# Optimization experiments

Hardware: AMD Instinct MI355X
Metric: run time of the kernel (lower is better)

## Reference

```python
import jax, jax.numpy as jnp
import numpy as np

LENS = 0.4
DECAY = 0.2
THRESH = 0.2
LOG_SIG_MIN, LOG_SIG_MAX = -20.0, 2.0

# Surrogate-gradient spike: forward is heaviside, backward is rectangular window |x|<lens
@jax.custom_vjp
def act_fun(x):
    return (x > 0.0).astype(x.dtype)

def _act_fwd(x):
    return act_fun(x), x

def _act_bwd(x, g):
    return (g * (jnp.abs(x) < LENS).astype(g.dtype),)

act_fun.defvjp(_act_fwd, _act_bwd)


def _xavier(k, shape):
    fan_out, fan_in = shape
    lim = float(np.sqrt(6.0 / (fan_in + fan_out)))
    return jax.random.uniform(k, shape, jnp.float32, -lim, lim)


def setup_inputs() -> dict:
    key = jax.random.key(0)
    ks = jax.random.split(key, 9)
    B, IN, H, A = 4096, 512, 2048, 32
    return {
        "state": jax.random.normal(ks[0], (B, 5, IN), jnp.float32),
        "W_lif": _xavier(ks[1], (H, IN)), "b_lif": jnp.zeros((H,), jnp.float32),
        "W11": _xavier(ks[2], (H, H)), "b11": jnp.zeros((H,), jnp.float32),
        "W12": _xavier(ks[3], (H, H)), "b12": jnp.zeros((H,), jnp.float32),
        "W21": _xavier(ks[4], (H, H)), "b21": jnp.zeros((H,), jnp.float32),
        "W22": _xavier(ks[5], (H, H)), "b22": jnp.zeros((H,), jnp.float32),
        "Wm": _xavier(ks[6], (A, H)), "bm": jnp.zeros((A,), jnp.float32),
        "Wls": _xavier(ks[7], (A, H)), "bls": jnp.zeros((A,), jnp.float32),
    }


def reference(state, W_lif, b_lif, W11, b11, W12, b12, W21, b21, W22, b22, Wm, bm, Wls, bls):
    x_seq = jnp.repeat(state, 3, axis=1)
    # precompute fc(x) for all steps in one GEMM: [B,15,H]
    fc = jnp.einsum('bti,hi->bth', x_seq, W_lif) + b_lif
    B, T, H = fc.shape

    def step(carry, fc_t):
        mem, spike = carry
        mem1 = mem * DECAY * (1.0 - spike) + fc_t
        spike1 = act_fun(mem1 - THRESH)
        return (mem1, spike1), spike1

    init = (jnp.zeros((B, H), fc.dtype), jnp.zeros((B, H), fc.dtype))
    _, spikes = jax.lax.scan(step, init, jnp.swapaxes(fc, 0, 1))  # [T,B,H]
    x = jnp.mean(spikes, axis=0)  # [B,H]

    x1 = jax.nn.relu(x @ W11.T + b11)
    x1 = jax.nn.relu(x1 @ W12.T + b12)
    mean = x1 @ Wm.T + bm

    x2 = jax.nn.relu(x @ W21.T + b21)
    x2 = jax.nn.relu(x2 @ W22.T + b22)
    log_std = jnp.clip(x2 @ Wls.T + bls, LOG_SIG_MIN, LOG_SIG_MAX)
    return mean, log_std
```

## Files before the change

### kernel.cpp

```cpp
#include <hip/hip_runtime.h>
#include <hip/hip_bf16.h>


typedef _Float16 f16;
using f32x4 = __attribute__((ext_vector_type(4))) float;
using f16x8 = __attribute__((ext_vector_type(8))) f16;

#define MFMA16(a, b, c) __builtin_amdgcn_mfma_f32_16x16x32_f16((a), (b), (c), 0, 0, 0)
#define VMW8()  asm volatile("s_waitcnt vmcnt(8)" ::: "memory")
#define VMW4()  asm volatile("s_waitcnt vmcnt(4)" ::: "memory")
#define VMW0()  asm volatile("s_waitcnt vmcnt(0)" ::: "memory")
#define LGKM0() asm volatile("s_waitcnt lgkmcnt(0)" ::: "memory")
#define BARRIER() __builtin_amdgcn_s_barrier()
#define SCHED0() __builtin_amdgcn_sched_barrier(0)

__device__ __forceinline__ void gload16(const void* g, void* l) {
  __builtin_amdgcn_global_load_lds(
      (const __attribute__((address_space(1))) unsigned int*)g,
      (__attribute__((address_space(3))) unsigned int*)l, 16, 0, 0);
}

__global__ __launch_bounds__(256) void cvt_kernel(
    const float* __restrict__ src, f16* __restrict__ dst, int n8)
{
  int i = blockIdx.x * 256 + threadIdx.x;
  if (i >= n8) return;
  const float4* s4 = (const float4*)src;
  float4 a = s4[(size_t)i * 2], b = s4[(size_t)i * 2 + 1];
  f16x8 d;
  d[0] = (f16)a.x; d[1] = (f16)a.y; d[2] = (f16)a.z; d[3] = (f16)a.w;
  d[4] = (f16)b.x; d[5] = (f16)b.y; d[6] = (f16)b.z; d[7] = (f16)b.w;
  *(f16x8*)(dst + (size_t)i * 8) = d;
}

__global__ __launch_bounds__(256) void cvt2_kernel(
    const float* __restrict__ s0, const float* __restrict__ s1,
    f16* __restrict__ d0, f16* __restrict__ d1, int n8each)
{
  int i = blockIdx.x * 256 + threadIdx.x;
  const float* src = (i < n8each) ? s0 : s1;
  f16* dst = (i < n8each) ? d0 : d1;
  int k = (i < n8each) ? i : i - n8each;
  if (k >= n8each) return;
  const float4* s4 = (const float4*)src;
  float4 a = s4[(size_t)k * 2], b = s4[(size_t)k * 2 + 1];
  f16x8 d;
  d[0] = (f16)a.x; d[1] = (f16)a.y; d[2] = (f16)a.z; d[3] = (f16)a.w;
  d[4] = (f16)b.x; d[5] = (f16)b.y; d[6] = (f16)b.z; d[7] = (f16)b.w;
  *(f16x8*)(dst + (size_t)k * 8) = d;
}

__global__ __launch_bounds__(512, 1) void lif256_kernel(
    const f16* __restrict__ S,
    const f16* __restrict__ W,
    const float* __restrict__ bl,
    f16* __restrict__ X)
{
  __shared__ alignas(16) f16 lds[4][128 * 64];

  const int tid = threadIdx.x, wid = tid >> 6, lane = tid & 63;
  const int wg = ((int)blockIdx.x % 8) * 64 + (int)blockIdx.x / 8;
  const int bn = wg & 15, bm = wg >> 4;
  const int b0 = bm * 128, h0 = bn * 128;
  const int wr0 = (wid >> 2) * 64, wc0 = (wid & 3) * 32;
  const int fr = lane & 15, fq = lane >> 4;
  const int sr = tid >> 3, scb = (tid & 7) * 16;

  f32x4 acc[4][2] = {};
  float mem[4][2][4] = {};
  float cnt[4][2][4] = {};

  auto STAGE = [&](int slot, int g) {
    const int s = g >> 3, k0 = (g & 7) * 64;
#pragma unroll
    for (int l = 0; l < 2; ++l) {
      const int row = l * 64 + sr;
      const int c2 = scb ^ ((row & 7) << 4);
      gload16(S + ((size_t)(b0 + row) * 5 + s) * 512 + k0 + (c2 >> 1),
              &lds[slot][l * 4096 + tid * 8]);
    }
#pragma unroll
    for (int l = 0; l < 2; ++l) {
      const int row = l * 64 + sr;
      const int c2 = scb ^ ((row & 7) << 4);
      gload16(W + (size_t)(h0 + row) * 512 + k0 + (c2 >> 1),
              &lds[2 + slot][l * 4096 + tid * 8]);
    }
  };

  auto LDA_ = [&](int slot, int mf, int ks) -> f16x8 {
    const int row = wr0 + mf * 16 + fr;
    const int c = (ks * 64 + fq * 16) ^ ((row & 7) << 4);
    return *(const f16x8*)&lds[slot][row * 64 + (c >> 1)];
  };
  auto LDB_ = [&](int slot, int nf, int ks) -> f16x8 {
    const int row = wc0 + nf * 16 + fr;
    const int c = (ks * 64 + fq * 16) ^ ((row & 7) << 4);
    return *(const f16x8*)&lds[2 + slot][row * 64 + (c >> 1)];
  };

  const float bias[2] = { bl[h0 + wc0 + fr], bl[h0 + wc0 + 16 + fr] };

  STAGE(0, 0);
  STAGE(1, 1);
  VMW4();
  BARRIER();
  SCHED0();

  for (int g = 0; g < 40; ++g) {
    const int slot = g & 1;

    f16x8 b[2][2], a[4][2];
#pragma unroll
    for (int nf = 0; nf < 2; ++nf) {
      b[nf][0] = LDB_(slot, nf, 0);
      b[nf][1] = LDB_(slot, nf, 1);
    }
#pragma unroll
    for (int mf = 0; mf < 4; ++mf) {
      a[mf][0] = LDA_(slot, mf, 0);
      a[mf][1] = LDA_(slot, mf, 1);
    }

    __builtin_amdgcn_s_setprio(1);
#pragma unroll
    for (int mf = 0; mf < 4; ++mf)
#pragma unroll
      for (int nf = 0; nf < 2; ++nf) {
        acc[mf][nf] = MFMA16(a[mf][0], b[nf][0], acc[mf][nf]);
        acc[mf][nf] = MFMA16(a[mf][1], b[nf][1], acc[mf][nf]);
      }
    __builtin_amdgcn_s_setprio(0);

    if ((g & 7) == 7) {
#pragma unroll
      for (int mf = 0; mf < 4; ++mf)
#pragma unroll
        for (int nf = 0; nf < 2; ++nf) {
#pragma unroll
          for (int r = 0; r < 4; ++r) {
            const float fc = acc[mf][nf][r] + bias[nf];
            float m = mem[mf][nf][r], c = cnt[mf][nf][r];
#pragma unroll
            for (int j = 0; j < 3; ++j) {
              m = ((m > 0.2f) ? 0.f : m * 0.2f) + fc;
              c += (m > 0.2f) ? 1.f : 0.f;
            }
            mem[mf][nf][r] = m; cnt[mf][nf][r] = c;
          }
          acc[mf][nf] = f32x4{0.f, 0.f, 0.f, 0.f};
        }
    }

    LGKM0();
    BARRIER();
    SCHED0();
    if (g + 2 < 40) {
      STAGE(slot, g + 2);
      SCHED0();
      VMW4();
    } else if (g + 1 < 40) {
      VMW0();
    }
    BARRIER();
    SCHED0();
  }

#pragma unroll
  for (int nf = 0; nf < 2; ++nf) {
    const int col = h0 + wc0 + nf * 16 + fr;
#pragma unroll
    for (int mf = 0; mf < 4; ++mf) {
      const int row0 = b0 + wr0 + mf * 16 + fq * 4;
#pragma unroll
      for (int r = 0; r < 4; ++r)
        X[(size_t)(row0 + r) * 2048 + col] = (f16)(cnt[mf][nf][r] / 15.0f);
    }
  }
}

__global__ __launch_bounds__(512, 2) void trunk256_kernel(
    const f16* __restrict__ A0, const f16* __restrict__ A1, int lda,
    const f16* __restrict__ W0, const f16* __restrict__ W1,
    const float* __restrict__ bb0, const float* __restrict__ bb1,
    f16* __restrict__ C0, f16* __restrict__ C1, int ldc,
    int nbm, int nbn_half, int K)
{
  __shared__ alignas(16) f16 lds[4][256 * 64];

  const int tid = threadIdx.x, wid = tid >> 6, lane = tid & 63;
  const int nwg = nbm * nbn_half * 2, q8 = nwg / 8;
  const int wg = ((int)blockIdx.x % 8) * q8 + (int)blockIdx.x / 8;
  const int bmi = wg % nbm, t = wg / nbm;
  const int half = (t >= nbn_half);
  const f16* Ap = half ? A1 : A0;
  const f16* Wp = half ? W1 : W0;
  const float* bias = half ? bb1 : bb0;
  f16* C = half ? C1 : C0;
  const int bm0 = bmi * 256;
  const int bn0 = (half ? t - nbn_half : t) * 256;

  const int wr0 = (wid >> 2) * 128, wc0 = (wid & 3) * 64;
  const int fr = lane & 15, fq = lane >> 4;
  const int sr = tid >> 3, scb = (tid & 7) * 16;

  f32x4 acc[8][4] = {};
  const int NT = K / 64;

  auto STAGE = [&](int slot, int kt) {
    const int k0 = kt * 64;
#pragma unroll
    for (int l = 0; l < 4; ++l) {
      const int row = l * 64 + sr;
      const int c2 = scb ^ ((row & 7) << 4);
      gload16(Ap + (size_t)(bm0 + row) * lda + k0 + (c2 >> 1),
              &lds[slot][l * 4096 + tid * 8]);
    }
#pragma unroll
    for (int l = 0; l < 4; ++l) {
      const int row = l * 64 + sr;
      const int c2 = scb ^ ((row & 7) << 4);
      gload16(Wp + (size_t)(bn0 + row) * K + k0 + (c2 >> 1),
              &lds[2 + slot][l * 4096 + tid * 8]);
    }
  };

  auto LDA_ = [&](int slot, int mf, int ks) -> f16x8 {
    const int row = wr0 + mf * 16 + fr;
    const int c = (ks * 64 + fq * 16) ^ ((row & 7) << 4);
    return *(const f16x8*)&lds[slot][row * 64 + (c >> 1)];
  };
  auto LDB_ = [&](int slot, int nf, int ks) -> f16x8 {
    const int row = wc0 + nf * 16 + fr;
    const int c = (ks * 64 + fq * 16) ^ ((row & 7) << 4);
    return *(const f16x8*)&lds[2 + slot][row * 64 + (c >> 1)];
  };

  STAGE(0, 0);
  STAGE(1, 1);
  VMW8();
  BARRIER();
  SCHED0();

  for (int kt = 0; kt < NT; ++kt) {
    const int slot = kt & 1;

    f16x8 b[4][2];
#pragma unroll
    for (int nf = 0; nf < 4; ++nf) {
      b[nf][0] = LDB_(slot, nf, 0);
      b[nf][1] = LDB_(slot, nf, 1);
    }
    f16x8 a0[2][2], a1[2][2];
#pragma unroll
    for (int i = 0; i < 2; ++i) {
      a0[i][0] = LDA_(slot, i, 0);
      a0[i][1] = LDA_(slot, i, 1);
    }

    auto QUAD = [&](int mbase, f16x8 (&a)[2][2]) {
      __builtin_amdgcn_s_setprio(1);
#pragma unroll
      for (int nf = 0; nf < 4; ++nf) {
        acc[mbase][nf]     = MFMA16(a[0][0], b[nf][0], acc[mbase][nf]);
        acc[mbase][nf]     = MFMA16(a[0][1], b[nf][1], acc[mbase][nf]);
        acc[mbase + 1][nf] = MFMA16(a[1][0], b[nf][0], acc[mbase + 1][nf]);
        acc[mbase + 1][nf] = MFMA16(a[1][1], b[nf][1], acc[mbase + 1][nf]);
      }
      __builtin_amdgcn_s_setprio(0);
    };

#pragma unroll
    for (int i = 0; i < 2; ++i) { a1[i][0] = LDA_(slot, 2 + i, 0); a1[i][1] = LDA_(slot, 2 + i, 1); }
    QUAD(0, a0);
#pragma unroll
    for (int i = 0; i < 2; ++i) { a0[i][0] = LDA_(slot, 4 + i, 0); a0[i][1] = LDA_(slot, 4 + i, 1); }
    QUAD(2, a1);
#pragma unroll
    for (int i = 0; i < 2; ++i) { a1[i][0] = LDA_(slot, 6 + i, 0); a1[i][1] = LDA_(slot, 6 + i, 1); }
    QUAD(4, a0);
    QUAD(6, a1);

    LGKM0();
    BARRIER();
    SCHED0();
    if (kt + 2 < NT) {
      STAGE(slot, kt + 2);
      SCHED0();
      VMW8();
    } else if (kt + 1 < NT) {
      VMW0();
    }
    BARRIER();
    SCHED0();
  }

#pragma unroll
  for (int nf = 0; nf < 4; ++nf) {
    const int col = bn0 + wc0 + nf * 16 + fr;
    const float bv = bias[col];
#pragma unroll
    for (int m = 0; m < 8; ++m) {
      const int row0 = bm0 + wr0 + m * 16 + fq * 4;
#pragma unroll
      for (int r = 0; r < 4; ++r) {
        float v = fmaxf(acc[m][nf][r] + bv, 0.f);
        C[(size_t)(row0 + r) * ldc + col] = (f16)v;
      }
    }
  }
}

__global__ __launch_bounds__(256) void head_kernel(
    const f16* __restrict__ H1, const f16* __restrict__ H2,
    const f16* __restrict__ Wm, const float* __restrict__ bm,
    const f16* __restrict__ Wls, const float* __restrict__ bls,
    float* __restrict__ OUT, int M, int K)
{
  const int tid = threadIdx.x, wid = tid >> 6, lane = tid & 63;
  const int m0 = blockIdx.x * 64 + wid * 16;
  const int kb = (lane >> 4) * 8, fr = lane & 15, fq = lane >> 4;

  f32x4 a1[2] = {}, a2[2] = {};
  for (int k0 = 0; k0 < K; k0 += 32) {
    f16x8 f1 = *(const f16x8*)&H1[(size_t)(m0 + fr) * K + k0 + kb];
    f16x8 f2 = *(const f16x8*)&H2[(size_t)(m0 + fr) * K + k0 + kb];
#pragma unroll
    for (int n = 0; n < 2; ++n) {
      f16x8 wm = *(const f16x8*)&Wm[(size_t)(n * 16 + fr) * K + k0 + kb];
      f16x8 wl = *(const f16x8*)&Wls[(size_t)(n * 16 + fr) * K + k0 + kb];
      a1[n] = MFMA16(f1, wm, a1[n]);
      a2[n] = MFMA16(f2, wl, a2[n]);
    }
  }

#pragma unroll
  for (int n = 0; n < 2; ++n) {
    const int col = n * 16 + fr;
    const float bvm = bm[col];
    const float bvl = bls[col];
#pragma unroll
    for (int r = 0; r < 4; ++r) {
      const int row = m0 + fq * 4 + r;
      OUT[(size_t)row * 32 + col] = a1[n][r] + bvm;
      float lv = a2[n][r] + bvl;
      OUT[(size_t)M * 32 + (size_t)row * 32 + col] = fminf(fmaxf(lv, -20.f), 2.f);
    }
  }
}

extern "C" void kernel_launch(void* const* d_in, const int* in_sizes, int n_in,
                              void* d_out, int out_size, void* d_ws, size_t ws_size,
                              hipStream_t stream) {
  const float* state = (const float*)d_in[0];
  const float* W_lif = (const float*)d_in[1];
  const float* b_lif = (const float*)d_in[2];
  const float* W11   = (const float*)d_in[3];
  const float* b11   = (const float*)d_in[4];
  const float* W12   = (const float*)d_in[5];
  const float* b12   = (const float*)d_in[6];
  const float* W21   = (const float*)d_in[7];
  const float* b21   = (const float*)d_in[8];
  const float* W22   = (const float*)d_in[9];
  const float* b22   = (const float*)d_in[10];
  const float* Wm    = (const float*)d_in[11];
  const float* bm    = (const float*)d_in[12];
  const float* Wls   = (const float*)d_in[13];
  const float* bls   = (const float*)d_in[14];
  float* out = (float*)d_out;

  const int B = 4096, IN = 512, H = 2048;
  char* ws = (char*)d_ws;
  f16* x    = (f16*)(ws);
  f16* h1   = (f16*)(ws + 16777216);
  f16* h2   = (f16*)(ws + 33554432);
  f16* s16  = (f16*)(ws + 50331648);
  f16* wl16 = (f16*)(ws + 71303168);
  f16* w11h = (f16*)(ws + 50331648);
  f16* w21h = (f16*)(ws + 58720256);
  f16* h22  = (f16*)(ws + 50331648);
  f16* w12h = (f16*)(ws + 67108864);
  f16* w22h = (f16*)(ws + 75497472);
  f16* wmh  = (f16*)(ws + 67108864);
  f16* wlsh = (f16*)(ws + 67239936);
  f16* h12  = x;

  cvt_kernel<<<(B * 5 * IN / 8) / 256, 256, 0, stream>>>(state, s16, B * 5 * IN / 8);
  cvt_kernel<<<(H * IN / 8) / 256, 256, 0, stream>>>(W_lif, wl16, H * IN / 8);

  lif256_kernel<<<512, 512, 0, stream>>>(s16, wl16, b_lif, x);

  cvt2_kernel<<<2 * (H * H / 8) / 256, 256, 0, stream>>>(W11, W21, w11h, w21h, H * H / 8);
  trunk256_kernel<<<256, 512, 0, stream>>>(x, x, H, w11h, w21h, b11, b21,
                                           h1, h2, H, 16, 8, H);

  cvt2_kernel<<<2 * (H * H / 8) / 256, 256, 0, stream>>>(W12, W22, w12h, w22h, H * H / 8);
  trunk256_kernel<<<256, 512, 0, stream>>>(h1, h2, H, w12h, w22h, b12, b22,
                                           h12, h22, H, 16, 8, H);

  cvt2_kernel<<<2 * (32 * H / 8) / 256, 256, 0, stream>>>(Wm, Wls, wmh, wlsh, 32 * H / 8);
  head_kernel<<<B / 64, 256, 0, stream>>>(h12, h22, wmh, bm, wlsh, bls, out, B, H);
}
```

Measured before the change: 285.0 us.

## Interleave LDS fragment loads with MFMA phases and issue prefetch before last compute

Both the LIF GEMM kernel and the trunk GEMM kernel now split each K-tile into phases. Each phase loads a few A fragments from LDS, synchronises the block with a barrier, and then runs its MFMAs. The next tile's global-to-LDS STAGE is issued before the final MFMA phase rather than after all compute, so global loads overlap the remaining math. Register pressure drops because fewer fragments are live at once, but the extra block barriers per iteration add synchronisation cost and may serialise the waves.

```diff
diff --git a/kernel.cpp b/kernel.cpp
--- a/kernel.cpp
+++ b/kernel.cpp
@@ -107,28 +107,49 @@
   BARRIER();
   SCHED0();
 
+#pragma unroll 2
   for (int g = 0; g < 40; ++g) {
     const int slot = g & 1;
 
-    f16x8 b[2][2], a[4][2];
+    f16x8 b[2][2], a[2][2];
 #pragma unroll
     for (int nf = 0; nf < 2; ++nf) {
       b[nf][0] = LDB_(slot, nf, 0);
       b[nf][1] = LDB_(slot, nf, 1);
     }
 #pragma unroll
-    for (int mf = 0; mf < 4; ++mf) {
-      a[mf][0] = LDA_(slot, mf, 0);
-      a[mf][1] = LDA_(slot, mf, 1);
-    }
-
+    for (int i = 0; i < 2; ++i) {
+      a[i][0] = LDA_(slot, i, 0);
+      a[i][1] = LDA_(slot, i, 1);
+    }
+    BARRIER(); LGKM0(); SCHED0();
     __builtin_amdgcn_s_setprio(1);
 #pragma unroll
-    for (int mf = 0; mf < 4; ++mf)
+    for (int i = 0; i < 2; ++i)
 #pragma unroll
       for (int nf = 0; nf < 2; ++nf) {
-        acc[mf][nf] = MFMA16(a[mf][0], b[nf][0], acc[mf][nf]);
-        acc[mf][nf] = MFMA16(a[mf][1], b[nf][1], acc[mf][nf]);
+        acc[i][nf] = MFMA16(a[i][0], b[nf][0], acc[i][nf]);
+        acc[i][nf] = MFMA16(a[i][1], b[nf][1], acc[i][nf]);
+      }
+    __builtin_amdgcn_s_setprio(0);
+    BARRIER();
+
+#pragma unroll
+    for (int i = 0; i < 2; ++i) {
+      a[i][0] = LDA_(slot, 2 + i, 0);
+      a[i][1] = LDA_(slot, 2 + i, 1);
+    }
+    LGKM0(); SCHED0();
+    BARRIER();
+    if (g + 2 < 40) STAGE(slot, g + 2);
+    SCHED0();
+    __builtin_amdgcn_s_setprio(1);
+#pragma unroll
+    for (int i = 0; i < 2; ++i)
+#pragma unroll
+      for (int nf = 0; nf < 2; ++nf) {
+        acc[2 + i][nf] = MFMA16(a[i][0], b[nf][0], acc[2 + i][nf]);
+        acc[2 + i][nf] = MFMA16(a[i][1], b[nf][1], acc[2 + i][nf]);
       }
     __builtin_amdgcn_s_setprio(0);
 
@@ -152,16 +173,8 @@
         }
     }
 
-    LGKM0();
-    BARRIER();
-    SCHED0();
-    if (g + 2 < 40) {
-      STAGE(slot, g + 2);
-      SCHED0();
-      VMW4();
-    } else if (g + 1 < 40) {
-      VMW0();
-    }
+    if (g + 2 < 40)      { VMW4(); }
+    else if (g + 1 < 40) { VMW0(); }
     BARRIER();
     SCHED0();
   }
@@ -244,21 +257,9 @@
 
   for (int kt = 0; kt < NT; ++kt) {
     const int slot = kt & 1;
-
-    f16x8 b[4][2];
-#pragma unroll
-    for (int nf = 0; nf < 4; ++nf) {
-      b[nf][0] = LDB_(slot, nf, 0);
-      b[nf][1] = LDB_(slot, nf, 1);
-    }
-    f16x8 a0[2][2], a1[2][2];
-#pragma unroll
-    for (int i = 0; i < 2; ++i) {
-      a0[i][0] = LDA_(slot, i, 0);
-      a0[i][1] = LDA_(slot, i, 1);
-    }
-
-    auto QUAD = [&](int mbase, f16x8 (&a)[2][2]) {
+    f16x8 b[4][2], a[2][2];
+
+    auto QUAD = [&](int mbase) {
       __builtin_amdgcn_s_setprio(1);
 #pragma unroll
       for (int nf = 0; nf < 4; ++nf) {
@@ -271,26 +272,37 @@
     };
 
 #pragma unroll
-    for (int i = 0; i < 2; ++i) { a1[i][0] = LDA_(slot, 2 + i, 0); a1[i][1] = LDA_(slot, 2 + i, 1); }
-    QUAD(0, a0);
-#pragma unroll
-    for (int i = 0; i < 2; ++i) { a0[i][0] = LDA_(slot, 4 + i, 0); a0[i][1] = LDA_(slot, 4 + i, 1); }
-    QUAD(2, a1);
-#pragma unroll
-    for (int i = 0; i < 2; ++i) { a1[i][0] = LDA_(slot, 6 + i, 0); a1[i][1] = LDA_(slot, 6 + i, 1); }
-    QUAD(4, a0);
-    QUAD(6, a1);
-
-    LGKM0();
-    BARRIER();
+    for (int nf = 0; nf < 4; ++nf) {
+      b[nf][0] = LDB_(slot, nf, 0);
+      b[nf][1] = LDB_(slot, nf, 1);
+    }
+#pragma unroll
+    for (int i = 0; i < 2; ++i) { a[i][0] = LDA_(slot, i, 0); a[i][1] = LDA_(slot, i, 1); }
+    BARRIER(); LGKM0(); SCHED0();
+    QUAD(0);
+    BARRIER();
+
+#pragma unroll
+    for (int i = 0; i < 2; ++i) { a[i][0] = LDA_(slot, 2 + i, 0); a[i][1] = LDA_(slot, 2 + i, 1); }
+    BARRIER(); LGKM0(); SCHED0();
+    QUAD(2);
+    BARRIER();
+
+#pragma unroll
+    for (int i = 0; i < 2; ++i) { a[i][0] = LDA_(slot, 4 + i, 0); a[i][1] = LDA_(slot, 4 + i, 1); }
+    BARRIER(); LGKM0(); SCHED0();
+    QUAD(4);
+    BARRIER();
+
+#pragma unroll
+    for (int i = 0; i < 2; ++i) { a[i][0] = LDA_(slot, 6 + i, 0); a[i][1] = LDA_(slot, 6 + i, 1); }
+    LGKM0(); SCHED0();
+    BARRIER();
+    if (kt + 2 < NT) STAGE(slot, kt + 2);
     SCHED0();
-    if (kt + 2 < NT) {
-      STAGE(slot, kt + 2);
-      SCHED0();
-      VMW8();
-    } else if (kt + 1 < NT) {
-      VMW0();
-    }
+    QUAD(6);
+    if (kt + 2 < NT)      { VMW8(); }
+    else if (kt + 1 < NT) { VMW0(); }
     BARRIER();
     SCHED0();
   }
```

Result: no change. 290.6 us (+2.0%).
